# Performance work log

Measured on AMD Instinct MI355X. Metric: run time of the kernel, lower is better.

## Reference

```python
import jax, jax.numpy as jnp
import numpy as np
import math

IN_DIM = 2048
OUT_DIM = 1152
SEQ_LEN = 8
WAY = 5
SHOT = 5
N_QUERIES = 100
MAX_LEN = int(SEQ_LEN * 1.5)
PE_SCALE = 0.1


def make_pe():
    pe = np.zeros((MAX_LEN, IN_DIM), dtype=np.float32)
    position = np.arange(0, MAX_LEN)[:, None].astype(np.float32)
    div_term = np.exp(np.arange(0, IN_DIM, 2).astype(np.float32) * -(math.log(10000.0) / IN_DIM))
    pe[:, 0::2] = np.sin(position * div_term) * PE_SCALE
    pe[:, 1::2] = np.cos(position * div_term) * PE_SCALE
    return jnp.asarray(pe)


def setup_inputs() -> dict:
    key = jax.random.key(0)
    ks = jax.random.split(key, 12)
    support_set = jax.random.normal(ks[0], (WAY * SHOT, SEQ_LEN, IN_DIM), dtype=jnp.float32)
    queries = jax.random.normal(ks[1], (N_QUERIES, SEQ_LEN, IN_DIM), dtype=jnp.float32)
    # labels: each class 0..WAY-1 appears SHOT times (sorted)
    support_labels = jnp.sort(jnp.arange(WAY * SHOT) % WAY)
    s = 1.0 / math.sqrt(IN_DIM)
    def lin(k):
        kw, kb = jax.random.split(k)
        W = jax.random.uniform(kw, (OUT_DIM, IN_DIM), minval=-s, maxval=s, dtype=jnp.float32)
        b = jax.random.uniform(kb, (OUT_DIM,), minval=-s, maxval=s, dtype=jnp.float32)
        return W, b
    sk_W, sk_b = lin(ks[2])
    sv_W, sv_b = lin(ks[3])
    qk_W, qk_b = lin(ks[4])
    qv_W, qv_b = lin(ks[5])
    return {
        "support_set": support_set,
        "support_labels": support_labels,
        "queries": queries,
        "sk_W": sk_W, "sk_b": sk_b,
        "sv_W": sv_W, "sv_b": sv_b,
        "qk_W": qk_W, "qk_b": qk_b,
        "qv_W": qv_W, "qv_b": qv_b,
        "ln_k_g": jnp.ones((OUT_DIM,), jnp.float32),
        "ln_k_b": jnp.zeros((OUT_DIM,), jnp.float32),
        "pe_table": make_pe(),
    }


def layer_norm(x, g, b, eps=1e-5):
    mu = jnp.mean(x, axis=-1, keepdims=True)
    var = jnp.var(x, axis=-1, keepdims=True)
    return (x - mu) / jnp.sqrt(var + eps) * g + b


def reference(support_set, support_labels, queries, sk_W, sk_b, sv_W, sv_b,
              qk_W, qk_b, qv_W, qv_b, ln_k_g, ln_k_b, pe_table):
    n_q, L, _ = queries.shape
    support_set = support_set + pe_table[None, :L]
    queries = queries + pe_table[None, :L]

    s_ks = layer_norm(support_set @ sk_W.T + sk_b, ln_k_g, ln_k_b)  # [S, L, D]
    q_ks = layer_norm(queries @ qk_W.T + qk_b, ln_k_g, ln_k_b)      # [Q, L, D]
    s_vs = support_set @ sv_W.T + sv_b                               # [S, L, D]
    q_vs = queries @ qv_W.T + qv_b                                   # [Q, L, D]

    D = q_ks.shape[-1]
    # group support by class: labels are sorted with equal shots per class
    k_bs = support_set.shape[0] // WAY
    class_k = s_ks.reshape(WAY, k_bs, L, D)   # [C, k, L, D]
    class_v = s_vs.reshape(WAY, k_bs, L, D)

    # scores: [C, Q, L(query), k*L(support)]
    scores = jnp.einsum('qld,ckmd->cqlkm', q_ks, class_k) / math.sqrt(D)
    scores = scores.reshape(WAY, n_q, L, k_bs * L)
    attn = jax.nn.softmax(scores, axis=-1)  # softmax over support frames per query frame
    attn = attn.reshape(WAY, n_q, L, k_bs, L).transpose(0, 1, 3, 2, 4)  # [C,Q,k,L,L]
    proto = jnp.einsum('cqklm,ckmd->cqld', attn, class_v)  # sum over k folded in

    diff = q_vs[None] - proto  # [C, Q, L, D]
    distance = jnp.sum(diff * diff, axis=(-2, -1)) / math.sqrt(D * L)  # [C, Q]
    return -distance.T  # [Q, C]
```

## Files before the change

### kernel.cpp

```cpp
#include <hip/hip_runtime.h>
#include <hip/hip_bf16.h>
#include <math.h>

#define WAY     5
#define NQ      100
#define SEQL    8
#define IN_DIM  2048
#define OUT_DIM 1152
#define QROWS   800
#define SROWS   200
#define QPAD    896
#define SPAD    256

#define OFF_SKB  0
#define OFF_SVB  1152
#define OFF_QKB  2304
#define OFF_QVB  3456
#define OFF_LNG  4608
#define OFF_LNB  5760
#define OFF_RSQ  6912
#define F32_END  7808

#define U_AQ   0
#define U_AS   (U_AQ  + QPAD*IN_DIM)
#define U_QKB  (U_AS  + SPAD*IN_DIM)
#define U_QVB  (U_QKB + QPAD*OUT_DIM)
#define U_SKB  (U_QVB + QPAD*OUT_DIM)
#define U_SVB  (U_SKB + SPAD*OUT_DIM)
#define SPSZ   (2048*SPAD)
#define U_SP   (U_SVB + SPAD*OUT_DIM)

typedef __attribute__((ext_vector_type(8))) short short8;
typedef __attribute__((ext_vector_type(4))) float f32x4;

__device__ __forceinline__ float bf2f(unsigned short u) {
    return __uint_as_float(((unsigned int)u) << 16);
}
__device__ __forceinline__ unsigned short f2bf(float f) {
    unsigned int u = __float_as_uint(f);
    return (unsigned short)((u + 0x7fffu + ((u >> 16) & 1u)) >> 16);
}
__device__ __forceinline__ bool sniff_bf16(const void* lng) {
    return *((const unsigned int*)lng) != 0x3F800000u;
}
__device__ __forceinline__ float load_s(const void* p, long idx, bool bf) {
    if (bf) return bf2f(((const unsigned short*)p)[idx]);
    return ((const float*)p)[idx];
}
__device__ __forceinline__ float4 load_v4(const void* p, long idx, bool bf) {
    if (bf) {
        ushort4 v = *((const ushort4*)((const unsigned short*)p + idx));
        return make_float4(bf2f(v.x), bf2f(v.y), bf2f(v.z), bf2f(v.w));
    }
    return *((const float4*)((const float*)p + idx));
}
__device__ __forceinline__ void gl_lds16(const unsigned short* g, unsigned short* l) {
    __builtin_amdgcn_global_load_lds(
        (const __attribute__((address_space(1))) unsigned int*)g,
        (__attribute__((address_space(3))) unsigned int*)l,
        16, 0, 0);
}
__device__ __forceinline__ void pack8(unsigned short* dst, float4 a, float4 b) {
    union { unsigned short us[8]; short8 v; } u;
    u.us[0] = f2bf(a.x); u.us[1] = f2bf(a.y); u.us[2] = f2bf(a.z); u.us[3] = f2bf(a.w);
    u.us[4] = f2bf(b.x); u.us[5] = f2bf(b.y); u.us[6] = f2bf(b.z); u.us[7] = f2bf(b.w);
    *(short8*)dst = u.v;
}

__global__ void stage_kernel(const void* support, const void* queries,
                             const void* skb, const void* svb,
                             const void* qkb, const void* qvb,
                             const void* lng, const void* lnb,
                             const void* pe, float* ws) {
    const bool bf = sniff_bf16(lng);
    unsigned short* ub = (unsigned short*)(ws + F32_END);
    const int tid = blockIdx.x * blockDim.x + threadIdx.x;
    const int stride = gridDim.x * blockDim.x;

    for (int i = tid; i < OUT_DIM; i += stride) {
        ws[OFF_SKB + i] = load_s(skb, i, bf);
        ws[OFF_SVB + i] = load_s(svb, i, bf);
        ws[OFF_QKB + i] = load_s(qkb, i, bf);
        ws[OFF_QVB + i] = load_s(qvb, i, bf);
        ws[OFF_LNG + i] = load_s(lng, i, bf);
        ws[OFF_LNB + i] = load_s(lnb, i, bf);
    }
    for (int i = tid; i < QPAD * (IN_DIM / 4); i += stride) {
        const int row = i >> 9, kc = (i & 511) * 4;
        ushort4 o;
        if (row < QROWS) {
            float4 v = load_v4(queries, (long)row * IN_DIM + kc, bf);
            const float4 p = load_v4(pe, (long)(row & 7) * IN_DIM + kc, bf);
            o.x = f2bf(v.x + p.x); o.y = f2bf(v.y + p.y);
            o.z = f2bf(v.z + p.z); o.w = f2bf(v.w + p.w);
        } else o = make_ushort4(0, 0, 0, 0);
        *(ushort4*)&ub[U_AQ + (long)row * IN_DIM + kc] = o;
    }
    for (int i = tid; i < SPAD * (IN_DIM / 4); i += stride) {
        const int row = i >> 9, kc = (i & 511) * 4;
        ushort4 o;
        if (row < SROWS) {
            float4 v = load_v4(support, (long)row * IN_DIM + kc, bf);
            const float4 p = load_v4(pe, (long)(row & 7) * IN_DIM + kc, bf);
            o.x = f2bf(v.x + p.x); o.y = f2bf(v.y + p.y);
            o.z = f2bf(v.z + p.z); o.w = f2bf(v.w + p.w);
        } else o = make_ushort4(0, 0, 0, 0);
        *(ushort4*)&ub[U_AS + (long)row * IN_DIM + kc] = o;
    }
}

__global__ __launch_bounds__(256) void proj_mfma(
        const void* skW, const void* svW, const void* qkW, const void* qvW,
        const void* lng, float* ws) {
    const bool is_bf = sniff_bf16(lng);
    unsigned short* ub = (unsigned short*)(ws + F32_END);

    const int jj = (blockIdx.x & 7) * 81 + (blockIdx.x >> 3);

    int job, nx, my;
    if (jj < 504) { job = jj / 252; const int r = jj % 252; my = r % 14; nx = r / 14; }
    else { const int t2 = jj - 504; job = 2 + t2 / 72; const int r = t2 % 72; my = r % 4; nx = r / 4; }

    const unsigned short* A = (job < 2) ? (ub + U_AQ) : (ub + U_AS);
    const void* Wv = (job == 0) ? qkW : (job == 1) ? qvW : (job == 2) ? skW : svW;
    unsigned short* outb = (job == 0) ? ub + U_QKB : (job == 1) ? ub + U_QVB
                         : (job == 2) ? ub + U_SKB : ub + U_SVB;
    const float* bias = ws + ((job == 0) ? OFF_QKB : (job == 1) ? OFF_QVB
                            : (job == 2) ? OFF_SKB : OFF_SVB);

    const int r0 = my * 64, n0 = nx * 64;

    __shared__ unsigned short Als[2][64 * 32];
    __shared__ unsigned short Bls[2][64 * 32];

    const int t = threadIdx.x, w = t >> 6, l = t & 63;
    const int wr = w >> 1, wc = w & 1;
    const int fm = l & 15, fq = l >> 4;
    const int srow = l >> 2, schunk = (l & 3) * 8;

    const unsigned short* Ag = A + (size_t)(r0 + w * 16 + srow) * IN_DIM + schunk;
    const int lofs = (w * 16) * 32;
    const int d = lofs + l * 8;

    f32x4 acc[2][2] = {};

#define MFMA_CORE(BUF)                                                          \
    {                                                                           \
        short8 af[2], bff[2];                                                   \
        _Pragma("unroll")                                                       \
        for (int i = 0; i < 2; ++i)                                             \
            af[i] = *(const short8*)&Als[BUF][(wr * 32 + i * 16 + fm) * 32 + fq * 8]; \
        _Pragma("unroll")                                                       \
        for (int j = 0; j < 2; ++j)                                             \
            bff[j] = *(const short8*)&Bls[BUF][(wc * 32 + j * 16 + fm) * 32 + fq * 8]; \
        _Pragma("unroll")                                                       \
        for (int i = 0; i < 2; ++i)                                             \
            _Pragma("unroll")                                                   \
            for (int j = 0; j < 2; ++j)                                         \
                acc[i][j] = __builtin_amdgcn_mfma_f32_16x16x32_bf16(            \
                    af[i], bff[j], acc[i][j], 0, 0, 0);                         \
    }

    if (is_bf) {
        const unsigned short* Bg = (const unsigned short*)Wv
            + (size_t)(n0 + w * 16 + srow) * IN_DIM + schunk;
        gl_lds16(Ag, &Als[0][lofs]);
        gl_lds16(Bg, &Bls[0][lofs]);
        __syncthreads();
        int cur = 0;
        for (int k0 = 0; k0 < IN_DIM; k0 += 32) {
            const int nxt = cur ^ 1;
            if (k0 + 32 < IN_DIM) {
                gl_lds16(Ag + k0 + 32, &Als[nxt][lofs]);
                gl_lds16(Bg + k0 + 32, &Bls[nxt][lofs]);
            }
            MFMA_CORE(cur)
            __syncthreads();
            cur = nxt;
        }
    } else {
        const float* Bgf = (const float*)Wv
            + (size_t)(n0 + w * 16 + srow) * IN_DIM + schunk;
        {
            const float4 x0 = *(const float4*)(Bgf);
            const float4 x1 = *(const float4*)(Bgf + 4);
            pack8(&Bls[0][d], x0, x1);
            gl_lds16(Ag, &Als[0][lofs]);
            __syncthreads();
        }
        int cur = 0;
        for (int k0 = 0; k0 < IN_DIM; k0 += 32) {
            const int nxt = cur ^ 1;
            float4 x0, x1;
            const bool more = (k0 + 32 < IN_DIM);
            if (more) {
                x0 = *(const float4*)(Bgf + k0 + 32);
                x1 = *(const float4*)(Bgf + k0 + 36);
                gl_lds16(Ag + k0 + 32, &Als[nxt][lofs]);
            }
            MFMA_CORE(cur)
            if (more) pack8(&Bls[nxt][d], x0, x1);
            __syncthreads();
            cur = nxt;
        }
    }
#undef MFMA_CORE

#pragma unroll
    for (int j = 0; j < 2; ++j) {
        const int col = n0 + wc * 32 + j * 16 + fm;
        const float bv = bias[col];
#pragma unroll
        for (int i = 0; i < 2; ++i) {
            const int rb = r0 + wr * 32 + i * 16 + fq * 4;
            const f32x4 v = acc[i][j];
#pragma unroll
            for (int r = 0; r < 4; ++r)
                outb[(size_t)(rb + r) * OUT_DIM + col] = f2bf(v[r] + bv);
        }
    }
}

__global__ __launch_bounds__(256) void finish_kernel(float* ws) {
    const int row = blockIdx.x;
    unsigned short* ub = (unsigned short*)(ws + F32_END);
    const int tid = threadIdx.x;
    __shared__ float xs[OUT_DIM];
    __shared__ float red[8];

    unsigned short* rp;
    int mode, qrow = 0;
    if (row < 896)       { rp = ub + U_QKB + (size_t)row * OUT_DIM; mode = 0; }
    else if (row < 1152) { rp = ub + U_SKB + (size_t)(row - 896) * OUT_DIM; mode = 0; }
    else                 { rp = ub + U_QVB + (size_t)(row - 1152) * OUT_DIM; mode = 1; qrow = row - 1152; }

    float s = 0.f, s2 = 0.f;
    for (int i = tid; i < OUT_DIM / 8; i += 256) {
        const short8 u = *(const short8*)(rp + i * 8);
#pragma unroll
        for (int k = 0; k < 8; ++k) {
            const float v = bf2f((unsigned short)u[k]);
            s += v;
            s2 = fmaf(v, v, s2);
            if (mode == 0) xs[i * 8 + k] = v;
        }
    }
    for (int o = 32; o > 0; o >>= 1) {
        s  += __shfl_down(s,  o, 64);
        s2 += __shfl_down(s2, o, 64);
    }
    if ((tid & 63) == 0) { red[tid >> 6] = s; red[4 + (tid >> 6)] = s2; }
    __syncthreads();

    if (mode == 0) {
        const float S  = red[0] + red[1] + red[2] + red[3];
        const float S2 = red[4] + red[5] + red[6] + red[7];
        const float mu = S * (1.0f / OUT_DIM);
        const float var = S2 * (1.0f / OUT_DIM) - mu * mu;
        const float rs = rsqrtf(var + 1e-5f);
        const float* g = ws + OFF_LNG;
        const float* bn = ws + OFF_LNB;
        for (int i = tid; i < OUT_DIM; i += 256)
            rp[i] = f2bf((xs[i] - mu) * rs * g[i] + bn[i]);
    } else if (tid == 0) {
        ws[OFF_RSQ + qrow] = red[4] + red[5] + red[6] + red[7];
    }
}

__global__ __launch_bounds__(256) void pair_mfma(float* ws) {
    unsigned short* ub = (unsigned short*)(ws + F32_END);
    const int job = blockIdx.z >> 2;
    const int chunk = blockIdx.z & 3;
    if (job >= 3) return;
    if (job == 2 && blockIdx.y >= 4) return;

    const unsigned short* A;
    const unsigned short* B;
    int rowbase;
    if (job == 0)      { A = ub + U_QKB; B = ub + U_SKB; rowbase = 0; }
    else if (job == 1) { A = ub + U_QVB; B = ub + U_SVB; rowbase = 896; }
    else               { A = ub + U_SVB; B = ub + U_SVB; rowbase = 1792; }
    unsigned short* out = ub + U_SP + (size_t)chunk * SPSZ + (size_t)rowbase * SPAD;

    const int r0 = blockIdx.y * 64;
    const int n0 = blockIdx.x * 64;
    const int kbeg = chunk * 288;

    __shared__ unsigned short Als[2][64 * 32];
    __shared__ unsigned short Bls[2][64 * 32];

    const int t = threadIdx.x, w = t >> 6, l = t & 63;
    const int wr = w >> 1, wc = w & 1;
    const int fm = l & 15, fq = l >> 4;
    const int srow = l >> 2, schunk = (l & 3) * 8;

    const unsigned short* Ag = A + (size_t)(r0 + w * 16 + srow) * OUT_DIM + schunk + kbeg;
    const unsigned short* Bg = B + (size_t)(n0 + w * 16 + srow) * OUT_DIM + schunk + kbeg;
    const int lofs = (w * 16) * 32;

    f32x4 acc[2][2] = {};

    gl_lds16(Ag, &Als[0][lofs]);
    gl_lds16(Bg, &Bls[0][lofs]);
    __syncthreads();

    int cur = 0;
    for (int k0 = 0; k0 < 288; k0 += 32) {
        const int nxt = cur ^ 1;
        if (k0 + 32 < 288) {
            gl_lds16(Ag + k0 + 32, &Als[nxt][lofs]);
            gl_lds16(Bg + k0 + 32, &Bls[nxt][lofs]);
        }

        short8 af[2], bff[2];
#pragma unroll
        for (int i = 0; i < 2; ++i)
            af[i] = *(const short8*)&Als[cur][(wr * 32 + i * 16 + fm) * 32 + fq * 8];
#pragma unroll
        for (int j = 0; j < 2; ++j)
            bff[j] = *(const short8*)&Bls[cur][(wc * 32 + j * 16 + fm) * 32 + fq * 8];
#pragma unroll
        for (int i = 0; i < 2; ++i)
#pragma unroll
            for (int j = 0; j < 2; ++j)
                acc[i][j] = __builtin_amdgcn_mfma_f32_16x16x32_bf16(
                    af[i], bff[j], acc[i][j], 0, 0, 0);

        __syncthreads();
        cur = nxt;
    }

#pragma unroll
    for (int j = 0; j < 2; ++j) {
        const int col = n0 + wc * 32 + j * 16 + fm;
#pragma unroll
        for (int i = 0; i < 2; ++i) {
            const int rb = r0 + wr * 32 + i * 16 + fq * 4;
            const f32x4 v = acc[i][j];
#pragma unroll
            for (int r = 0; r < 4; ++r)
                out[(size_t)(rb + r) * SPAD + col] = f2bf(v[r]);
        }
    }
}

__global__ __launch_bounds__(256) void final_kernel(const void* lng, float* ws, void* outp) {
    const bool bf = sniff_bf16(lng);
    const int c = blockIdx.x;
    const int q = blockIdx.y;
    unsigned short* ub = (unsigned short*)(ws + F32_END);
    const unsigned short* P = ub + U_SP;

    __shared__ float sS[SEQL][40];
    __shared__ float sT[SEQL][40];
    __shared__ float sA[SEQL][40];
    __shared__ float sG[40][41];
    __shared__ float red[4];

    const int tid = threadIdx.x;
    const float isd = 0.029462782549439483f;

    for (int i = tid; i < SEQL * 40; i += 256) {
        const int l = i / 40, j = i % 40;
        const size_t rs = (size_t)(q * SEQL + l) * SPAD + c * 40 + j;
        const size_t rt = (size_t)(896 + q * SEQL + l) * SPAD + c * 40 + j;
        float s = 0.f, t = 0.f;
#pragma unroll
        for (int p = 0; p < 4; ++p) {
            s += bf2f(P[(size_t)p * SPSZ + rs]);
            t += bf2f(P[(size_t)p * SPSZ + rt]);
        }
        sS[l][j] = s * isd;
        sT[l][j] = t;
    }
    for (int i = tid; i < 40 * 40; i += 256) {
        const int j = i / 40, j2 = i % 40;
        const size_t rg = (size_t)(1792 + c * 40 + j) * SPAD + c * 40 + j2;
        float g = 0.f;
#pragma unroll
        for (int p = 0; p < 4; ++p) g += bf2f(P[(size_t)p * SPSZ + rg]);
        sG[j][j2] = g;
    }
    __syncthreads();

    if (tid < SEQL) {
        const int l = tid;
        float m = -1e30f;
        for (int j = 0; j < 40; ++j) m = fmaxf(m, sS[l][j]);
        float sum = 0.f;
        for (int j = 0; j < 40; ++j) { float e = __expf(sS[l][j] - m); sA[l][j] = e; sum += e; }
        const float inv = 1.0f / sum;
        for (int j = 0; j < 40; ++j) sA[l][j] *= inv;
    }
    __syncthreads();

    float part = 0.f;
    for (int i = tid; i < SEQL * 40; i += 256) {
        const int l = i / 40, j = i % 40;
        float gs = 0.f;
        for (int j2 = 0; j2 < 40; ++j2) gs = fmaf(sG[j][j2], sA[l][j2], gs);
        part += sA[l][j] * (gs - 2.0f * sT[l][j]);
    }
    for (int o = 32; o > 0; o >>= 1) part += __shfl_down(part, o, 64);
    if ((tid & 63) == 0) red[tid >> 6] = part;
    __syncthreads();

    if (tid == 0) {
        float qn = 0.f;
        for (int l = 0; l < SEQL; ++l) qn += ws[OFF_RSQ + q * SEQL + l];
        const float tot = red[0] + red[1] + red[2] + red[3] + qn;
        const float r = -(tot * (1.0f / 96.0f));
        if (bf) ((__hip_bfloat16*)outp)[q * WAY + c] = __float2bfloat16(r);
        else    ((float*)outp)[q * WAY + c] = r;
    }
}

extern "C" void kernel_launch(void* const* d_in, const int* in_sizes, int n_in,
                              void* d_out, int out_size, void* d_ws, size_t ws_size,
                              hipStream_t stream) {
    const void* support = d_in[0];
    const void* queries = d_in[2];
    const void* skW = d_in[3];  const void* skb = d_in[4];
    const void* svW = d_in[5];  const void* svb = d_in[6];
    const void* qkW = d_in[7];  const void* qkb = d_in[8];
    const void* qvW = d_in[9];  const void* qvb = d_in[10];
    const void* lng = d_in[11]; const void* lnb = d_in[12];
    const void* pe  = d_in[13];
    float* ws = (float*)d_ws;

    stage_kernel<<<dim3(512), dim3(256), 0, stream>>>(
        support, queries, skb, svb, qkb, qvb, lng, lnb, pe, ws);
    proj_mfma<<<dim3(648), dim3(256), 0, stream>>>(skW, svW, qkW, qvW, lng, ws);
    finish_kernel<<<dim3(2048), dim3(256), 0, stream>>>(ws);
    pair_mfma<<<dim3(4, 14, 12), dim3(256), 0, stream>>>(ws);
    final_kernel<<<dim3(WAY, NQ), dim3(256), 0, stream>>>(lng, ws, d_out);
}
```

Measured before the change: 180.0 us.

## Pre-convert fp32 weights to bf16 and use 4-stage async LDS pipeline

```diff
diff --git a/kernel.cpp b/kernel.cpp
--- a/kernel.cpp
+++ b/kernel.cpp
@@ -29,6 +29,7 @@
 #define U_SVB  (U_SKB + SPAD*OUT_DIM)
 #define SPSZ   (2048*SPAD)
 #define U_SP   (U_SVB + SPAD*OUT_DIM)
+#define U_W    (U_SP + 4*SPSZ)
 
 typedef __attribute__((ext_vector_type(8))) short short8;
 typedef __attribute__((ext_vector_type(4))) float f32x4;
@@ -60,14 +61,12 @@
         (__attribute__((address_space(3))) unsigned int*)l,
         16, 0, 0);
 }
-__device__ __forceinline__ void pack8(unsigned short* dst, float4 a, float4 b) {
-    union { unsigned short us[8]; short8 v; } u;
-    u.us[0] = f2bf(a.x); u.us[1] = f2bf(a.y); u.us[2] = f2bf(a.z); u.us[3] = f2bf(a.w);
-    u.us[4] = f2bf(b.x); u.us[5] = f2bf(b.y); u.us[6] = f2bf(b.z); u.us[7] = f2bf(b.w);
-    *(short8*)dst = u.v;
-}
+
+#define VMWAIT(N) asm volatile("s_waitcnt vmcnt(" #N ")" ::: "memory")
 
 __global__ void stage_kernel(const void* support, const void* queries,
+                             const void* skW, const void* svW,
+                             const void* qkW, const void* qvW,
                              const void* skb, const void* svb,
                              const void* qkb, const void* qvb,
                              const void* lng, const void* lnb,
@@ -107,6 +106,21 @@
         } else o = make_ushort4(0, 0, 0, 0);
         *(ushort4*)&ub[U_AS + (long)row * IN_DIM + kc] = o;
     }
+    if (!bf) {
+        const float* Wsrc[4] = {(const float*)qkW, (const float*)qvW,
+                                (const float*)skW, (const float*)svW};
+        for (int j = 0; j < 4; ++j) {
+            unsigned short* dst = ub + U_W + (long)j * OUT_DIM * IN_DIM;
+            const float* src = Wsrc[j];
+            for (int i = tid; i < OUT_DIM * (IN_DIM / 4); i += stride) {
+                const long e = (long)i * 4;
+                const float4 v = *(const float4*)(src + e);
+                ushort4 o;
+                o.x = f2bf(v.x); o.y = f2bf(v.y); o.z = f2bf(v.z); o.w = f2bf(v.w);
+                *(ushort4*)&dst[e] = o;
+            }
+        }
+    }
 }
 
 __global__ __launch_bounds__(256) void proj_mfma(
@@ -122,7 +136,6 @@
     else { const int t2 = jj - 504; job = 2 + t2 / 72; const int r = t2 % 72; my = r % 4; nx = r / 4; }
 
     const unsigned short* A = (job < 2) ? (ub + U_AQ) : (ub + U_AS);
-    const void* Wv = (job == 0) ? qkW : (job == 1) ? qvW : (job == 2) ? skW : svW;
     unsigned short* outb = (job == 0) ? ub + U_QKB : (job == 1) ? ub + U_QVB
                          : (job == 2) ? ub + U_SKB : ub + U_SVB;
     const float* bias = ws + ((job == 0) ? OFF_QKB : (job == 1) ? OFF_QVB
@@ -130,8 +143,8 @@
 
     const int r0 = my * 64, n0 = nx * 64;
 
-    __shared__ unsigned short Als[2][64 * 32];
-    __shared__ unsigned short Bls[2][64 * 32];
+    __shared__ unsigned short Als[4][64 * 32];
+    __shared__ unsigned short Bls[4][64 * 32];
 
     const int t = threadIdx.x, w = t >> 6, l = t & 63;
     const int wr = w >> 1, wc = w & 1;
@@ -139,10 +152,23 @@
     const int srow = l >> 2, schunk = (l & 3) * 8;
 
     const unsigned short* Ag = A + (size_t)(r0 + w * 16 + srow) * IN_DIM + schunk;
+    const unsigned short* Bg;
+    if (is_bf) {
+        const void* Wv = (job == 0) ? qkW : (job == 1) ? qvW : (job == 2) ? skW : svW;
+        Bg = (const unsigned short*)Wv + (size_t)(n0 + w * 16 + srow) * IN_DIM + schunk;
+    } else {
+        Bg = ub + U_W + (size_t)job * OUT_DIM * IN_DIM
+           + (size_t)(n0 + w * 16 + srow) * IN_DIM + schunk;
+    }
     const int lofs = (w * 16) * 32;
-    const int d = lofs + l * 8;
 
     f32x4 acc[2][2] = {};
+
+#define PSTAGE(tt) do {                                   \
+        const int b_ = (tt) & 3;                          \
+        gl_lds16(Ag + (size_t)(tt) * 32, &Als[b_][lofs]); \
+        gl_lds16(Bg + (size_t)(tt) * 32, &Bls[b_][lofs]); \
+    } while (0)
 
 #define MFMA_CORE(BUF)                                                          \
     {                                                                           \
@@ -161,49 +187,19 @@
                     af[i], bff[j], acc[i][j], 0, 0, 0);                         \
     }
 
-    if (is_bf) {
-        const unsigned short* Bg = (const unsigned short*)Wv
-            + (size_t)(n0 + w * 16 + srow) * IN_DIM + schunk;
-        gl_lds16(Ag, &Als[0][lofs]);
-        gl_lds16(Bg, &Bls[0][lofs]);
-        __syncthreads();
-        int cur = 0;
-        for (int k0 = 0; k0 < IN_DIM; k0 += 32) {
-            const int nxt = cur ^ 1;
-            if (k0 + 32 < IN_DIM) {
-                gl_lds16(Ag + k0 + 32, &Als[nxt][lofs]);
-                gl_lds16(Bg + k0 + 32, &Bls[nxt][lofs]);
-            }
-            MFMA_CORE(cur)
-            __syncthreads();
-            cur = nxt;
-        }
-    } else {
-        const float* Bgf = (const float*)Wv
-            + (size_t)(n0 + w * 16 + srow) * IN_DIM + schunk;
-        {
-            const float4 x0 = *(const float4*)(Bgf);
-            const float4 x1 = *(const float4*)(Bgf + 4);
-            pack8(&Bls[0][d], x0, x1);
-            gl_lds16(Ag, &Als[0][lofs]);
-            __syncthreads();
-        }
-        int cur = 0;
-        for (int k0 = 0; k0 < IN_DIM; k0 += 32) {
-            const int nxt = cur ^ 1;
-            float4 x0, x1;
-            const bool more = (k0 + 32 < IN_DIM);
-            if (more) {
-                x0 = *(const float4*)(Bgf + k0 + 32);
-                x1 = *(const float4*)(Bgf + k0 + 36);
-                gl_lds16(Ag + k0 + 32, &Als[nxt][lofs]);
-            }
-            MFMA_CORE(cur)
-            if (more) pack8(&Bls[nxt][d], x0, x1);
-            __syncthreads();
-            cur = nxt;
-        }
-    }
+    PSTAGE(0); PSTAGE(1); PSTAGE(2);
+
+    const int T = IN_DIM / 32;
+    for (int kt = 0; kt < T; ++kt) {
+        if (kt <= T - 3)      VMWAIT(4);
+        else if (kt == T - 2) VMWAIT(2);
+        else                  VMWAIT(0);
+        __builtin_amdgcn_s_barrier();
+        __builtin_amdgcn_sched_barrier(0);
+        if (kt + 3 < T) PSTAGE(kt + 3);
+        MFMA_CORE(kt & 3)
+    }
+#undef PSTAGE
 #undef MFMA_CORE
 
 #pragma unroll
@@ -286,8 +282,8 @@
     const int n0 = blockIdx.x * 64;
     const int kbeg = chunk * 288;
 
-    __shared__ unsigned short Als[2][64 * 32];
-    __shared__ unsigned short Bls[2][64 * 32];
+    __shared__ unsigned short Als[4][64 * 32];
+    __shared__ unsigned short Bls[4][64 * 32];
 
     const int t = threadIdx.x, w = t >> 6, l = t & 63;
     const int wr = w >> 1, wc = w & 1;
@@ -300,35 +296,39 @@
 
     f32x4 acc[2][2] = {};
 
-    gl_lds16(Ag, &Als[0][lofs]);
-    gl_lds16(Bg, &Bls[0][lofs]);
-    __syncthreads();
-
-    int cur = 0;
-    for (int k0 = 0; k0 < 288; k0 += 32) {
-        const int nxt = cur ^ 1;
-        if (k0 + 32 < 288) {
-            gl_lds16(Ag + k0 + 32, &Als[nxt][lofs]);
-            gl_lds16(Bg + k0 + 32, &Bls[nxt][lofs]);
-        }
-
+#define PSTAGE(tt) do {                                   \
+        const int b_ = (tt) & 3;                          \
+        gl_lds16(Ag + (size_t)(tt) * 32, &Als[b_][lofs]); \
+        gl_lds16(Bg + (size_t)(tt) * 32, &Bls[b_][lofs]); \
+    } while (0)
+
+    PSTAGE(0); PSTAGE(1); PSTAGE(2);
+
+    const int T = 9;
+    for (int kt = 0; kt < T; ++kt) {
+        if (kt <= T - 3)      VMWAIT(4);
+        else if (kt == T - 2) VMWAIT(2);
+        else                  VMWAIT(0);
+        __builtin_amdgcn_s_barrier();
+        __builtin_amdgcn_sched_barrier(0);
+        if (kt + 3 < T) PSTAGE(kt + 3);
+
+        const int buf = kt & 3;
         short8 af[2], bff[2];
 #pragma unroll
         for (int i = 0; i < 2; ++i)
-            af[i] = *(const short8*)&Als[cur][(wr * 32 + i * 16 + fm) * 32 + fq * 8];
+            af[i] = *(const short8*)&Als[buf][(wr * 32 + i * 16 + fm) * 32 + fq * 8];
 #pragma unroll
         for (int j = 0; j < 2; ++j)
-            bff[j] = *(const short8*)&Bls[cur][(wc * 32 + j * 16 + fm) * 32 + fq * 8];
+            bff[j] = *(const short8*)&Bls[buf][(wc * 32 + j * 16 + fm) * 32 + fq * 8];
 #pragma unroll
         for (int i = 0; i < 2; ++i)
 #pragma unroll
             for (int j = 0; j < 2; ++j)
                 acc[i][j] = __builtin_amdgcn_mfma_f32_16x16x32_bf16(
                     af[i], bff[j], acc[i][j], 0, 0, 0);
-
-        __syncthreads();
-        cur = nxt;
-    }
+    }
+#undef PSTAGE
 
 #pragma unroll
     for (int j = 0; j < 2; ++j) {
@@ -429,7 +429,7 @@
     float* ws = (float*)d_ws;
 
     stage_kernel<<<dim3(512), dim3(256), 0, stream>>>(
-        support, queries, skb, svb, qkb, qvb, lng, lnb, pe, ws);
+        support, queries, skW, svW, qkW, qvW, skb, svb, qkb, qvb, lng, lnb, pe, ws);
     proj_mfma<<<dim3(648), dim3(256), 0, stream>>>(skW, svW, qkW, qvW, lng, ws);
     finish_kernel<<<dim3(2048), dim3(256), 0, stream>>>(ws);
     pair_mfma<<<dim3(4, 14, 12), dim3(256), 0, stream>>>(ws);
```

Result: faster. 168.0 us (-6.7%).
